# Optimization experiments

Measured on AMD Instinct MI355X. Metric: run time of the kernel, lower is better.

The kernel has to match this reference:

```python
import jax, jax.numpy as jnp
import numpy as np

N = 100000        # nodes
E = 1600000       # edges (avg degree 16)
D1, D2 = 512, 256 # omic feature dims
H = 64            # hidden_dim
C = 4             # num_classes


def setup_inputs() -> dict:
    key = jax.random.key(0)
    ks = jax.random.split(key, 13)
    s = 0.05  # param scale
    return {
        "x_omic1": jax.random.normal(ks[0], (N, D1), dtype=jnp.float32),
        "x_omic2": jax.random.normal(ks[1], (N, D2), dtype=jnp.float32),
        "edge_index": jax.random.randint(ks[2], (2, E), 0, N, dtype=jnp.int32),
        # GCNConv weights/biases, branch 1 (omic1)
        "W1a": jax.random.normal(ks[3], (D1, H), dtype=jnp.float32) * s,
        "b1a": jnp.zeros((H,), dtype=jnp.float32),
        "W2a": jax.random.normal(ks[4], (H, H), dtype=jnp.float32) * s,
        "b2a": jnp.zeros((H,), dtype=jnp.float32),
        # branch 2 (omic2)
        "W1b": jax.random.normal(ks[5], (D2, H), dtype=jnp.float32) * s,
        "b1b": jnp.zeros((H,), dtype=jnp.float32),
        "W2b": jax.random.normal(ks[6], (H, H), dtype=jnp.float32) * s,
        "b2b": jnp.zeros((H,), dtype=jnp.float32),
        # final classifier
        "Wfc": jax.random.normal(ks[7], (2 * H, C), dtype=jnp.float32) * s,
        "bfc": jnp.zeros((C,), dtype=jnp.float32),
    }


def reference(x_omic1, x_omic2, edge_index, W1a, b1a, W2a, b2a,
              W1b, b1b, W2b, b2b, Wfc, bfc):
    n = x_omic1.shape[0]
    # GCN normalization with self-loops: A_hat = A + I, norm = d^-1/2 d^-1/2
    loop = jnp.arange(n, dtype=edge_index.dtype)
    src = jnp.concatenate([edge_index[0], loop])
    dst = jnp.concatenate([edge_index[1], loop])
    deg = jax.ops.segment_sum(jnp.ones_like(src, dtype=x_omic1.dtype), dst,
                              num_segments=n)
    dinv = jnp.where(deg > 0, jax.lax.rsqrt(jnp.maximum(deg, 1.0)), 0.0)
    norm = dinv[src] * dinv[dst]  # [E+N]

    def gcn(x, W, b):
        h = x @ W                              # dense linear [n, H]
        msg = h[src] * norm[:, None]           # gather + scale
        return jax.ops.segment_sum(msg, dst, num_segments=n) + b

    # dropout is identity in eval mode
    x1 = jax.nn.elu(gcn(x_omic1, W1a, b1a))
    x1 = jax.nn.elu(gcn(x1, W2a, b2a))
    x2 = jax.nn.elu(gcn(x_omic2, W1b, b1b))
    x2 = jax.nn.elu(gcn(x2, W2b, b2b))
    x = jnp.concatenate([x1, x2], axis=1)      # [n, 2H]
    return x @ Wfc + bfc
```

## Files before the change

### kernel.cpp

```cpp
#include <hip/hip_runtime.h>
#include <hip/hip_bf16.h>
#include <math.h>


#define H 64
#define BCAP 16384

static inline int ceil_div(int a, int b) { return (a + b - 1) / b; }

typedef __attribute__((ext_vector_type(8))) short short8_t;
typedef __attribute__((ext_vector_type(4))) float f32x4;

__device__ inline unsigned short f2bf_rne(float f) {
    unsigned u = __float_as_uint(f);
    u += 0x7fffu + ((u >> 16) & 1u);
    return (unsigned short)(u >> 16);
}
__device__ inline unsigned pk_bf(float a, float b) {
    return (unsigned)f2bf_rne(a) | ((unsigned)f2bf_rne(b) << 16);
}
__device__ inline float2 bf2x(unsigned w) {
    float2 r;
    r.x = __uint_as_float(w << 16);
    r.y = __uint_as_float(w & 0xffff0000u);
    return r;
}
union V8 { uint4 u4; unsigned u[4]; short8_t s; };

__device__ inline void split_pack2(float a, float b, unsigned& hi, unsigned& lo) {
    union { __hip_bfloat162 h; unsigned u; } hp, lp;
    hp.h = __float22bfloat162_rn(make_float2(a, b));
    float fa = __uint_as_float(hp.u << 16);
    float fb = __uint_as_float(hp.u & 0xffff0000u);
    lp.h = __float22bfloat162_rn(make_float2(a - fa, b - fb));
    hi = hp.u;
    lo = lp.u;
}

__global__ __launch_bounds__(256) void bucket_scatter_kernel(
        const int* __restrict__ src, const int* __restrict__ dst,
        int* __restrict__ cursor, unsigned* __restrict__ bucketed,
        int E, int nbkt) {
    __shared__ int lcnt[512];
    __shared__ int lbase[512];
    const int t = threadIdx.x;
    for (int b = t; b < nbkt; b += 256) lcnt[b] = 0;
    __syncthreads();

    unsigned val[8];
    int bkt[8], lpos[8];
    const int e0 = blockIdx.x * 2048;
#pragma unroll
    for (int k = 0; k < 8; ++k) {
        int e = e0 + k * 256 + t;
        bkt[k] = -1;
        if (e < E) {
            int s = src[e];
            int d = dst[e];
            int b = d >> 8;
            val[k] = (unsigned)s | ((unsigned)(d & 255) << 17);
            bkt[k] = b;
            lpos[k] = atomicAdd(&lcnt[b], 1);
        }
    }
    __syncthreads();
    for (int b = t; b < nbkt; b += 256) {
        int c = lcnt[b];
        lbase[b] = c > 0 ? atomicAdd(&cursor[b], c) : 0;
    }
    __syncthreads();
#pragma unroll
    for (int k = 0; k < 8; ++k) {
        if (bkt[k] >= 0) {
            int p = lbase[bkt[k]] + lpos[k];
            if (p < BCAP)
                bucketed[(size_t)bkt[k] * BCAP + p] = val[k];
        }
    }
}

__global__ __launch_bounds__(256) void bucket_csr_kernel(
        const unsigned* __restrict__ bucketed, const int* __restrict__ cursor,
        int* __restrict__ csr_src, int* __restrict__ row_ptr,
        float* __restrict__ dinv, int N, int E) {
    __shared__ int dcnt[256];
    __shared__ int dbase[256];
    __shared__ int dcur[256];
    const int t = threadIdx.x;
    const int b = blockIdx.x;

    int part = 0;
    for (int i = t; i < b; i += 256) part += cursor[i];
    dbase[t] = part;
    __syncthreads();
#pragma unroll
    for (int off = 128; off > 0; off >>= 1) {
        if (t < off) dbase[t] += dbase[t + off];
        __syncthreads();
    }
    const int base = dbase[0];
    const int cnt = min(cursor[b], BCAP);
    const unsigned* bed = bucketed + (size_t)b * BCAP;
    if (b == 0 && t == 0) row_ptr[N] = E;

    dcnt[t] = 0;
    __syncthreads();
    for (int i = t; i < cnt; i += 256) {
        unsigned v = bed[i];
        atomicAdd(&dcnt[v >> 17], 1);
    }
    __syncthreads();
    int myc = dcnt[t];
    int acc = myc;
    dbase[t] = acc;
    __syncthreads();
#pragma unroll
    for (int off = 1; off < 256; off <<= 1) {
        int u = (t >= off) ? dbase[t - off] : 0;
        __syncthreads();
        dbase[t] += u;
        __syncthreads();
    }
    int excl = dbase[t] - myc;
    dcur[t] = excl;
    int node = b * 256 + t;
    if (node < N) {
        row_ptr[node] = base + excl;
        dinv[node] = rsqrtf((float)myc + 1.0f);
    }
    __syncthreads();
    for (int i = t; i < cnt; i += 256) {
        unsigned v = bed[i];
        int dl = v >> 17;
        int p = atomicAdd(&dcur[dl], 1);
        csr_src[base + p] = (int)(v & 0x1FFFFu);
    }
}

__global__ __launch_bounds__(256) void wfrag4_kernel(
        const float* __restrict__ Wa, uint4* __restrict__ fa,
        const float* __restrict__ Wb, uint4* __restrict__ fb,
        const float* __restrict__ Wc, uint4* __restrict__ fc,
        const float* __restrict__ Wd, uint4* __restrict__ fd,
        int* __restrict__ cursor) {
    const int bid = blockIdx.x;
    if (bid == 0) {
        cursor[threadIdx.x] = 0;
        cursor[threadIdx.x + 256] = 0;
    }
    const float* W;
    uint4* frag;
    int K, t;
    if (bid < 16)      { W = Wa; frag = fa; K = 512; t = bid * 256 + threadIdx.x; }
    else if (bid < 24) { W = Wb; frag = fb; K = 256; t = (bid - 16) * 256 + threadIdx.x; }
    else if (bid < 26) { W = Wc; frag = fc; K = 64;  t = (bid - 24) * 256 + threadIdx.x; }
    else               { W = Wd; frag = fd; K = 64;  t = (bid - 26) * 256 + threadIdx.x; }
    int total = (K >> 5) * 256;
    if (t >= total) return;
    int lane = t & 63, nt = (t >> 6) & 3, ks = t >> 8;
    int nl = lane & 15, q = lane >> 4;
    float hi[8], lo[8];
#pragma unroll
    for (int j = 0; j < 8; ++j) {
        float w = W[(size_t)(ks * 32 + q * 8 + j) * 64 + nt * 16 + nl];
        unsigned hb = f2bf_rne(w);
        float hf = __uint_as_float(((unsigned)hb) << 16);
        hi[j] = hf;
        lo[j] = w - hf;
    }
    V8 vh, vl;
#pragma unroll
    for (int j = 0; j < 4; ++j) {
        vh.u[j] = pk_bf(hi[2 * j], hi[2 * j + 1]);
        vl.u[j] = pk_bf(lo[2 * j], lo[2 * j + 1]);
    }
    size_t base = (size_t)((ks * 4 + nt) * 2) * 64 + lane;
    frag[base] = vh.u4;
    frag[base + 64] = vl.u4;
}

__global__ __launch_bounds__(256) void gemm_l1_kernel(
        const float* __restrict__ XA, const uint4* __restrict__ wfA,
        unsigned* __restrict__ HA, int KA,
        const float* __restrict__ XB, const uint4* __restrict__ wfB,
        unsigned* __restrict__ HB, int KB,
        int M, int nblkA) {
    const float* X;
    const uint4* wf;
    unsigned* Hout;
    int K, blk;
    if ((int)blockIdx.x < nblkA) { X = XA; wf = wfA; Hout = HA; K = KA; blk = blockIdx.x; }
    else                         { X = XB; wf = wfB; Hout = HB; K = KB; blk = blockIdx.x - nblkA; }

    const int tid = threadIdx.x;
    const int w = tid >> 6, l = tid & 63;
    const int m = l & 15, q = l >> 4;
    const int wbase = blk * 128 + w * 32;

    const float* Xr[2];
#pragma unroll
    for (int s = 0; s < 2; ++s) {
        int row = wbase + s * 16 + m;
        int rowc = row < M ? row : M - 1;
        Xr[s] = X + (size_t)rowc * K;
    }

    f32x4 acc[2][4];
#pragma unroll
    for (int s = 0; s < 2; ++s)
#pragma unroll
        for (int nt = 0; nt < 4; ++nt) acc[s][nt] = (f32x4){0.f, 0.f, 0.f, 0.f};

    const int ksteps = K >> 5;
    for (int ks = 0; ks < ksteps; ++ks) {
        float4 xf[2][2];
#pragma unroll
        for (int s = 0; s < 2; ++s) {
            xf[s][0] = *(const float4*)&Xr[s][ks * 32 + q * 8];
            xf[s][1] = *(const float4*)&Xr[s][ks * 32 + q * 8 + 4];
        }
        const uint4* base = wf + (size_t)(ks * 4) * 2 * 64 + l;
        uint4 bh[4], bl[4];
#pragma unroll
        for (int nt = 0; nt < 4; ++nt) {
            bh[nt] = base[(size_t)(nt * 2) * 64];
            bl[nt] = base[(size_t)(nt * 2 + 1) * 64];
        }
#pragma unroll
        for (int s = 0; s < 2; ++s) {
            float xs[8] = {xf[s][0].x, xf[s][0].y, xf[s][0].z, xf[s][0].w,
                           xf[s][1].x, xf[s][1].y, xf[s][1].z, xf[s][1].w};
            V8 ah, al;
#pragma unroll
            for (int j = 0; j < 4; ++j)
                split_pack2(xs[2 * j], xs[2 * j + 1], ah.u[j], al.u[j]);
#pragma unroll
            for (int nt = 0; nt < 4; ++nt) {
                V8 vh, vl;
                vh.u4 = bh[nt];
                vl.u4 = bl[nt];
                acc[s][nt] = __builtin_amdgcn_mfma_f32_16x16x32_bf16(ah.s, vh.s, acc[s][nt], 0, 0, 0);
                acc[s][nt] = __builtin_amdgcn_mfma_f32_16x16x32_bf16(al.s, vh.s, acc[s][nt], 0, 0, 0);
                acc[s][nt] = __builtin_amdgcn_mfma_f32_16x16x32_bf16(ah.s, vl.s, acc[s][nt], 0, 0, 0);
            }
        }
    }

#pragma unroll
    for (int s = 0; s < 2; ++s) {
        const int rbase = wbase + s * 16 + q * 4;
#pragma unroll
        for (int nt = 0; nt < 4; ++nt) {
#pragma unroll
            for (int i = 0; i < 4; ++i) {
                float f = acc[s][nt][i];
                float fo = __shfl_xor(f, 1, 64);
                int r = rbase + i;
                if (((l & 1) == 0) && r < M)
                    Hout[(size_t)r * 32 + nt * 8 + (m >> 1)] = pk_bf(f, fo);
            }
        }
    }
}

__global__ __launch_bounds__(256) void gemm_l2_kernel(
        const uint4* __restrict__ XA, const uint4* __restrict__ wfA,
        unsigned* __restrict__ HA,
        const uint4* __restrict__ XB, const uint4* __restrict__ wfB,
        unsigned* __restrict__ HB,
        int M, int nblkA) {
    const uint4* Xb;
    const uint4* wf;
    unsigned* Hout;
    int blk;
    if ((int)blockIdx.x < nblkA) { Xb = XA; wf = wfA; Hout = HA; blk = blockIdx.x; }
    else                         { Xb = XB; wf = wfB; Hout = HB; blk = blockIdx.x - nblkA; }

    const int tid = threadIdx.x;
    const int w = tid >> 6, l = tid & 63;
    const int m = l & 15, q = l >> 4;
    const int tile = blk * 64 + w * 16;
    int row = tile + m;
    int rowc = row < M ? row : M - 1;

    f32x4 acc[4];
#pragma unroll
    for (int nt = 0; nt < 4; ++nt) acc[nt] = (f32x4){0.f, 0.f, 0.f, 0.f};

#pragma unroll
    for (int ks = 0; ks < 2; ++ks) {
        V8 av;
        av.u4 = Xb[(size_t)rowc * 8 + ks * 4 + q];
        const uint4* base = wf + (size_t)(ks * 4) * 2 * 64 + l;
#pragma unroll
        for (int nt = 0; nt < 4; ++nt) {
            V8 bh, bl;
            bh.u4 = base[(size_t)(nt * 2) * 64];
            bl.u4 = base[(size_t)(nt * 2 + 1) * 64];
            acc[nt] = __builtin_amdgcn_mfma_f32_16x16x32_bf16(av.s, bh.s, acc[nt], 0, 0, 0);
            acc[nt] = __builtin_amdgcn_mfma_f32_16x16x32_bf16(av.s, bl.s, acc[nt], 0, 0, 0);
        }
    }

    const int rbase = tile + q * 4;
#pragma unroll
    for (int nt = 0; nt < 4; ++nt) {
#pragma unroll
        for (int i = 0; i < 4; ++i) {
            float f = acc[nt][i];
            float fo = __shfl_xor(f, 1, 64);
            int r = rbase + i;
            if (((l & 1) == 0) && r < M)
                Hout[(size_t)r * 32 + nt * 8 + (m >> 1)] = pk_bf(f, fo);
        }
    }
}

__global__ __launch_bounds__(256) void agg2_kernel(const unsigned* __restrict__ h1,
                                                   const unsigned* __restrict__ h2,
                                                   const float* __restrict__ dinv,
                                                   const int* __restrict__ row_ptr,
                                                   const int* __restrict__ csr_src,
                                                   const float* __restrict__ b1,
                                                   const float* __restrict__ b2,
                                                   unsigned* __restrict__ o1,
                                                   unsigned* __restrict__ o2,
                                                   const float* __restrict__ Wfc,
                                                   const float* __restrict__ bfc,
                                                   float* __restrict__ out, int n) {
    const int tid  = threadIdx.x;
    const int lane = tid & 63;
    const int wave = tid >> 6;
    const int half = lane >> 5;
    const int l    = lane & 31;
    const int hb   = half << 5;
    const int node = blockIdx.x * 8 + wave * 2 + half;
    const bool active = (node < n);

    int r0 = 0, r1 = 0;
    float di = 0.f;
    if (active) { r0 = row_ptr[node]; r1 = row_ptr[node + 1]; di = dinv[node]; }
    const float di2 = di * di;
    const int rowoff = node * 32 + l;

    float2 acc1 = make_float2(0.f, 0.f), acc2 = make_float2(0.f, 0.f);
    if (active) {
        float2 s1 = bf2x(h1[rowoff]);
        float2 s2 = bf2x(h2[rowoff]);
        acc1.x = s1.x * di2; acc1.y = s1.y * di2;
        acc2.x = s2.x * di2; acc2.y = s2.y * di2;
    }

    for (int base = r0; base < r1; base += 32) {
        int cnt = r1 - base;
        if (cnt > 32) cnt = 32;
        int j = base + (l < cnt ? l : cnt - 1);
        int sj = csr_src[j];
        float dsj = dinv[sj];
#pragma unroll 4
        for (int t = 0; t < cnt; ++t) {
            int s    = __shfl(sj, hb | t, 64);
            float nr = __shfl(dsj, hb | t, 64) * di;
            float2 g1 = bf2x(h1[s * 32 + l]);
            float2 g2 = bf2x(h2[s * 32 + l]);
            acc1.x = fmaf(g1.x, nr, acc1.x);
            acc1.y = fmaf(g1.y, nr, acc1.y);
            acc2.x = fmaf(g2.x, nr, acc2.x);
            acc2.y = fmaf(g2.y, nr, acc2.y);
        }
    }

    float2 bv1 = ((const float2*)b1)[l];
    float2 bv2 = ((const float2*)b2)[l];
    float2 v1, v2;
    v1.x = acc1.x + bv1.x; v1.y = acc1.y + bv1.y;
    v2.x = acc2.x + bv2.x; v2.y = acc2.y + bv2.y;
    v1.x = v1.x > 0.f ? v1.x : (expf(v1.x) - 1.f);
    v1.y = v1.y > 0.f ? v1.y : (expf(v1.y) - 1.f);
    v2.x = v2.x > 0.f ? v2.x : (expf(v2.x) - 1.f);
    v2.y = v2.y > 0.f ? v2.y : (expf(v2.y) - 1.f);

    if (Wfc == nullptr) {
        if (active) {
            o1[rowoff] = pk_bf(v1.x, v1.y);
            o2[rowoff] = pk_bf(v2.x, v2.y);
        }
        return;
    }

    const float* Wp1 = &Wfc[(2 * l) * 4];
    const float* Wp2 = &Wfc[(H + 2 * l) * 4];
    float a[4];
#pragma unroll
    for (int c = 0; c < 4; ++c)
        a[c] = v1.x * Wp1[c] + v1.y * Wp1[4 + c] + v2.x * Wp2[c] + v2.y * Wp2[4 + c];
#pragma unroll
    for (int off = 16; off > 0; off >>= 1) {
#pragma unroll
        for (int c = 0; c < 4; ++c)
            a[c] += __shfl_down(a[c], off, 64);
    }
    if (l == 0 && active) {
#pragma unroll
        for (int c = 0; c < 4; ++c)
            out[(size_t)node * 4 + c] = a[c] + bfc[c];
    }
}

extern "C" void kernel_launch(void* const* d_in, const int* in_sizes, int n_in,
                              void* d_out, int out_size, void* d_ws, size_t ws_size,
                              hipStream_t stream) {
    const float* x_omic1 = (const float*)d_in[0];
    const float* x_omic2 = (const float*)d_in[1];
    const int*   eidx    = (const int*)d_in[2];
    const float* W1a = (const float*)d_in[3];
    const float* b1a = (const float*)d_in[4];
    const float* W2a = (const float*)d_in[5];
    const float* b2a = (const float*)d_in[6];
    const float* W1b = (const float*)d_in[7];
    const float* b1b = (const float*)d_in[8];
    const float* W2b = (const float*)d_in[9];
    const float* b2b = (const float*)d_in[10];
    const float* Wfc = (const float*)d_in[11];
    const float* bfc = (const float*)d_in[12];
    float* out = (float*)d_out;

    const int D1 = 512, D2 = 256;
    const int N = in_sizes[0] / D1;
    const int E = in_sizes[2] / 2;
    const int* src = eidx;
    const int* dst = eidx + E;
    const int nbkt = ceil_div(N, 256);

    size_t off = 0;
    auto alloc = [&](size_t elems) { size_t o = off; off += (elems + 3) & ~(size_t)3; return o; };
    float*    base_f = (float*)d_ws;
    int*      base_i = (int*)d_ws;
    unsigned* base_u = (unsigned*)d_ws;
    float*    dinv     = base_f + alloc(N);
    int*      row_ptr  = base_i + alloc(N + 1);
    int*      cursor   = base_i + alloc(512);
    unsigned* bucketed = base_u + alloc((size_t)nbkt * BCAP);
    int*      csr_src  = base_i + alloc(E);
    unsigned* h1bf     = base_u + alloc((size_t)N * 32);
    unsigned* h2bf     = base_u + alloc((size_t)N * 32);
    unsigned* x1bf     = base_u + alloc((size_t)N * 32);
    unsigned* x2bf     = base_u + alloc((size_t)N * 32);
    uint4*    wf1a = (uint4*)(base_u + alloc((D1 / 32) * 2 * 256 * 4));
    uint4*    wf1b = (uint4*)(base_u + alloc((D2 / 32) * 2 * 256 * 4));
    uint4*    wf2a = (uint4*)(base_u + alloc((H  / 32) * 2 * 256 * 4));
    uint4*    wf2b = (uint4*)(base_u + alloc((H  / 32) * 2 * 256 * 4));

    dim3 blk(256);
    dim3 grid_agg(ceil_div(N, 8));
    const int nblk = ceil_div(N, 64);
    const int nblkL1 = ceil_div(N, 128);

    wfrag4_kernel<<<28, blk, 0, stream>>>(W1a, wf1a, W1b, wf1b, W2a, wf2a,
                                          W2b, wf2b, cursor);
    bucket_scatter_kernel<<<ceil_div(E, 2048), blk, 0, stream>>>(src, dst, cursor,
                                                                 bucketed, E, nbkt);
    bucket_csr_kernel<<<nbkt, blk, 0, stream>>>(bucketed, cursor, csr_src,
                                                row_ptr, dinv, N, E);
    gemm_l1_kernel<<<2 * nblkL1, blk, 0, stream>>>(x_omic1, wf1a, h1bf, D1,
                                                   x_omic2, wf1b, h2bf, D2, N, nblkL1);
    agg2_kernel<<<grid_agg, blk, 0, stream>>>(h1bf, h2bf, dinv, row_ptr, csr_src,
                                              b1a, b1b, x1bf, x2bf,
                                              nullptr, nullptr, nullptr, N);
    gemm_l2_kernel<<<2 * nblk, blk, 0, stream>>>((const uint4*)x1bf, wf2a, h1bf,
                                                 (const uint4*)x2bf, wf2b, h2bf,
                                                 N, nblk);
    agg2_kernel<<<grid_agg, blk, 0, stream>>>(h1bf, h2bf, dinv, row_ptr, csr_src,
                                              b2a, b2b, nullptr, nullptr,
                                              Wfc, bfc, out, N);
}
```

Baseline: 688.9 us.

## Double-buffer layer-1 GEMM operands in LDS via async global-to-LDS loads

```diff
diff --git a/kernel.cpp b/kernel.cpp
--- a/kernel.cpp
+++ b/kernel.cpp
@@ -35,6 +35,13 @@
     lp.h = __float22bfloat162_rn(make_float2(a - fa, b - fb));
     hi = hp.u;
     lo = lp.u;
+}
+
+__device__ inline void async16(void* lds, const void* g) {
+    __builtin_amdgcn_global_load_lds(
+        (const __attribute__((address_space(1))) unsigned*)g,
+        (__attribute__((address_space(3))) unsigned*)lds,
+        16, 0, 0);
 }
 
 __global__ __launch_bounds__(256) void bucket_scatter_kernel(
@@ -185,6 +192,9 @@
         const float* __restrict__ XB, const uint4* __restrict__ wfB,
         unsigned* __restrict__ HB, int KB,
         int M, int nblkA) {
+    __shared__ __align__(16) unsigned xlds[2][4096];
+    __shared__ __align__(16) unsigned flds[2][2048];
+
     const float* X;
     const uint4* wf;
     unsigned* Hout;
@@ -195,14 +205,21 @@
     const int tid = threadIdx.x;
     const int w = tid >> 6, l = tid & 63;
     const int m = l & 15, q = l >> 4;
-    const int wbase = blk * 128 + w * 32;
-
-    const float* Xr[2];
-#pragma unroll
-    for (int s = 0; s < 2; ++s) {
-        int row = wbase + s * 16 + m;
-        int rowc = row < M ? row : M - 1;
-        Xr[s] = X + (size_t)rowc * K;
+    const int row0 = blk * 128;
+    const int ksteps = K >> 5;
+    const unsigned* wfu = (const unsigned*)wf;
+
+    const float* xsrc[4];
+    int xdst[4];
+#pragma unroll
+    for (int j = 0; j < 4; ++j) {
+        int c = w * 256 + j * 64 + l;
+        int r = c >> 3;
+        int sg = (c & 7) ^ (r & 7);
+        int row = row0 + r;
+        row = row < M ? row : M - 1;
+        xsrc[j] = X + (size_t)row * K + sg * 4;
+        xdst[j] = (w * 256 + j * 64) * 4;
     }
 
     f32x4 acc[2][4];
@@ -211,25 +228,31 @@
 #pragma unroll
         for (int nt = 0; nt < 4; ++nt) acc[s][nt] = (f32x4){0.f, 0.f, 0.f, 0.f};
 
-    const int ksteps = K >> 5;
-    for (int ks = 0; ks < ksteps; ++ks) {
-        float4 xf[2][2];
+    auto stage = [&](int b, int ks) {
+#pragma unroll
+        for (int j = 0; j < 4; ++j)
+            async16(&xlds[b][xdst[j]], xsrc[j] + ks * 32);
+#pragma unroll
+        for (int j = 0; j < 2; ++j) {
+            int c0 = w * 128 + j * 64;
+            async16(&flds[b][c0 * 4], wfu + ((size_t)ks * 512 + c0 + l) * 4);
+        }
+    };
+
+    auto compute = [&](int b) {
+        uint4 bh[4], bl[4];
+#pragma unroll
+        for (int nt = 0; nt < 4; ++nt) {
+            bh[nt] = *(const uint4*)&flds[b][((nt * 2) * 64 + l) * 4];
+            bl[nt] = *(const uint4*)&flds[b][((nt * 2 + 1) * 64 + l) * 4];
+        }
 #pragma unroll
         for (int s = 0; s < 2; ++s) {
-            xf[s][0] = *(const float4*)&Xr[s][ks * 32 + q * 8];
-            xf[s][1] = *(const float4*)&Xr[s][ks * 32 + q * 8 + 4];
-        }
-        const uint4* base = wf + (size_t)(ks * 4) * 2 * 64 + l;
-        uint4 bh[4], bl[4];
-#pragma unroll
-        for (int nt = 0; nt < 4; ++nt) {
-            bh[nt] = base[(size_t)(nt * 2) * 64];
-            bl[nt] = base[(size_t)(nt * 2 + 1) * 64];
-        }
-#pragma unroll
-        for (int s = 0; s < 2; ++s) {
-            float xs[8] = {xf[s][0].x, xf[s][0].y, xf[s][0].z, xf[s][0].w,
-                           xf[s][1].x, xf[s][1].y, xf[s][1].z, xf[s][1].w};
+            int r = w * 32 + s * 16 + m;
+            int sw = r & 7;
+            float4 x0 = *(const float4*)&xlds[b][(r * 8 + ((2 * q) ^ sw)) * 4];
+            float4 x1 = *(const float4*)&xlds[b][(r * 8 + ((2 * q + 1) ^ sw)) * 4];
+            float xs[8] = {x0.x, x0.y, x0.z, x0.w, x1.x, x1.y, x1.z, x1.w};
             V8 ah, al;
 #pragma unroll
             for (int j = 0; j < 4; ++j)
@@ -244,11 +267,22 @@
                 acc[s][nt] = __builtin_amdgcn_mfma_f32_16x16x32_bf16(ah.s, vl.s, acc[s][nt], 0, 0, 0);
             }
         }
-    }
+    };
+
+    stage(0, 0);
+    __syncthreads();
+    int buf = 0;
+    for (int ks = 0; ks + 1 < ksteps; ++ks) {
+        stage(buf ^ 1, ks + 1);
+        compute(buf);
+        __syncthreads();
+        buf ^= 1;
+    }
+    compute(buf);
 
 #pragma unroll
     for (int s = 0; s < 2; ++s) {
-        const int rbase = wbase + s * 16 + q * 4;
+        const int rbase = row0 + w * 32 + s * 16 + q * 4;
 #pragma unroll
         for (int nt = 0; nt < 4; ++nt) {
 #pragma unroll
```

Measured after the change: 675.2 us. 2.0% less time.
